# Optimization experiments

Measured on AMD Instinct MI355X. Metric: run time of the kernel, lower is better.

Reference implementation:

```python
import jax, jax.numpy as jnp
import numpy as np

N_TOTAL = 2_000_000   # total particles across all events
N_EVENTS = 20_000     # number of events (segments)
H = 64                # phi/rho hidden width
OUT = 10              # output classes


def _lin(x, W, b):
    # torch nn.Linear: y = x @ W.T + b
    return x @ W.T + b


def setup_inputs() -> dict:
    key = jax.random.key(0)
    ks = jax.random.split(key, 24)
    s = 0.1  # small init scale
    inp = {
        "values": jax.random.normal(ks[0], (N_TOTAL,), dtype=jnp.float32),
        "seg_ids": jnp.sort(jax.random.randint(ks[1], (N_TOTAL,), 0, N_EVENTS)),
        "p1w0": jax.random.normal(ks[2], (H, 1), dtype=jnp.float32) * s,
        "p1b0": jax.random.normal(ks[3], (H,), dtype=jnp.float32) * s,
        "p1w1": jax.random.normal(ks[4], (H, H), dtype=jnp.float32) * s,
        "p1b1": jax.random.normal(ks[5], (H,), dtype=jnp.float32) * s,
        "r1w0": jax.random.normal(ks[6], (H, H), dtype=jnp.float32) * s,
        "r1b0": jax.random.normal(ks[7], (H,), dtype=jnp.float32) * s,
        "r1w1": jax.random.normal(ks[8], (H, H), dtype=jnp.float32) * s,
        "r1b1": jax.random.normal(ks[9], (H,), dtype=jnp.float32) * s,
        "o1w": jax.random.normal(ks[10], (H, H), dtype=jnp.float32) * s,
        "o1b": jax.random.normal(ks[11], (H,), dtype=jnp.float32) * s,
        "p2w0": jax.random.normal(ks[12], (H, H), dtype=jnp.float32) * s,
        "p2b0": jax.random.normal(ks[13], (H,), dtype=jnp.float32) * s,
        "p2w1": jax.random.normal(ks[14], (H, H), dtype=jnp.float32) * s,
        "p2b1": jax.random.normal(ks[15], (H,), dtype=jnp.float32) * s,
        "r2w0": jax.random.normal(ks[16], (H, H), dtype=jnp.float32) * s,
        "r2b0": jax.random.normal(ks[17], (H,), dtype=jnp.float32) * s,
        "r2w1": jax.random.normal(ks[18], (H, H), dtype=jnp.float32) * s,
        "r2b1": jax.random.normal(ks[19], (H,), dtype=jnp.float32) * s,
        "o2w": jax.random.normal(ks[20], (OUT, H), dtype=jnp.float32) * s,
        "o2b": jax.random.normal(ks[21], (OUT,), dtype=jnp.float32) * s,
    }
    return inp


def reference(values, seg_ids, p1w0, p1b0, p1w1, p1b1, r1w0, r1b0, r1w1, r1b1,
              o1w, o1b, p2w0, p2b0, p2w1, p2b1, r2w0, r2b0, r2w1, r2b1, o2w, o2b):
    relu = jax.nn.relu
    # stage 1: phi1 on each scalar particle value -> [N, H]
    h = relu(_lin(values[:, None], p1w0, p1b0))
    h = relu(_lin(h, p1w1, p1b1))
    # jagged sum over particles within each event (the inner deepset sum)
    ev = jax.ops.segment_sum(h, seg_ids, num_segments=N_EVENTS)  # [E, H]
    # rho1 + output linear + activation per event
    ev = relu(_lin(ev, r1w0, r1b0))
    ev = relu(_lin(ev, r1w1, r1b1))
    ev = relu(_lin(ev, o1w, o1b))  # [E, H] (output_size of deepset1 = rho_sizes[-1])
    # stage 2: phi2 per event, sum over all events
    h2 = relu(_lin(ev, p2w0, p2b0))
    h2 = relu(_lin(h2, p2w1, p2b1))
    s2 = jnp.sum(h2, axis=0, keepdims=True)  # [1, H]
    r2 = relu(_lin(s2, r2w0, r2b0))
    r2 = relu(_lin(r2, r2w1, r2b1))
    out = _lin(r2, o2w, o2b)  # [1, OUT]
    return jax.nn.log_softmax(out, axis=1)
```

## Files before the change

kernel.cpp:

```cpp
#include <hip/hip_runtime.h>

#define NT 2000000
#define NE 20000
#define NT4 (NT / 4)
#define K1_BLOCKS 2048
#define K1_WAVES (K1_BLOCKS * 4)
#define K2_BLOCKS ((NE + 63) / 64)
#define NSEG 65
#define K0_BLOCKS ((NT4 + 255) / 256)

using half8  = __attribute__((ext_vector_type(8))) _Float16;
using half4v = __attribute__((ext_vector_type(4))) _Float16;
using f32x4  = __attribute__((ext_vector_type(4))) float;
using fvec4  = __attribute__((ext_vector_type(4))) float;

__device__ __forceinline__ half8 load_h8(const float* __restrict__ p) {
    fvec4 a = *(const fvec4*)p;
    fvec4 b = *(const fvec4*)(p + 4);
    half8 r;
#pragma unroll
    for (int e = 0; e < 4; e++) {
        r[e]     = (_Float16)a[e];
        r[e + 4] = (_Float16)b[e];
    }
    return r;
}

__global__ __launch_bounds__(256) void k0_fused(
    const int* __restrict__ seg, int* __restrict__ off, float* __restrict__ s2,
    int* __restrict__ counter,
    const float* __restrict__ w0, const float* __restrict__ b0,
    const float* __restrict__ w1, const float* __restrict__ b1,
    float* __restrict__ sorted_t, half4v* __restrict__ tabg) {
    if (blockIdx.x < NSEG) {
        __shared__ float tS[64], w0S[64], b0S[64], aS[64], cS[64];
        __shared__ int styleS[64], rankS[64];
        const int k = threadIdx.x;
        float t = 0.f; int rank = 0;
        if (k < 64) {
            const float w = w0[k], b = b0[k];
            int style;
            if (w != 0.f) { t = -b / w; style = (w > 0.f) ? 1 : 0; }
            else          { t = (b > 0.f) ? -INFINITY : INFINITY; style = 1; }
            tS[k] = t; w0S[k] = w; b0S[k] = b; styleS[k] = style;
        }
        __syncthreads();
        if (k < 64) {
            for (int i = 0; i < 64; i++) {
                const float ti = tS[i];
                rank += (ti < t || (ti == t && i < k)) ? 1 : 0;
            }
            rankS[k] = rank;
        }
        __syncthreads();
        if (k < 64) {
            if (blockIdx.x == 0) sorted_t[rank] = t;
            const int s = blockIdx.x;
            float a = 0.f, c = b1[k];
            for (int kk = 0; kk < 64; kk++) {
                const bool act = styleS[kk] ? (s > rankS[kk]) : (s <= rankS[kk]);
                if (act) {
                    const float wjk = w1[k * 64 + kk];
                    a = fmaf(wjk, w0S[kk], a);
                    c = fmaf(wjk, b0S[kk], c);
                }
            }
            aS[k] = a; cS[k] = c;
        }
        __syncthreads();
        if (k < 32) {
            const int s = blockIdx.x;
            tabg[s * 32 + k] = half4v{
                (_Float16)aS[2 * k],     (_Float16)cS[2 * k],
                (_Float16)aS[2 * k + 1], (_Float16)cS[2 * k + 1]};
        }
    }

    if (blockIdx.x == 0) {
        if (threadIdx.x < 64) s2[threadIdx.x] = 0.f;
        if (threadIdx.x == 64) *counter = 0;
    }
    const int g = blockIdx.x * 256 + threadIdx.x;
    if (g >= NT4) return;
    const int idx4 = g * 4;
    const int4 s = *(const int4*)(seg + idx4);
    int prev = (g == 0) ? -1 : seg[idx4 - 1];
    int vals[4] = {s.x, s.y, s.z, s.w};
#pragma unroll
    for (int k = 0; k < 4; k++) {
        const int cur = vals[k];
        if (cur != prev) {
            for (int e = prev + 1; e <= cur; ++e) off[e] = idx4 + k;
        }
        prev = cur;
    }
    if (idx4 + 3 == NT - 1) {
        for (int e = prev + 1; e <= NE; ++e) off[e] = NT;
    }
}

__global__ __launch_bounds__(256) void k1_phi1(
    const float* __restrict__ values, const int* __restrict__ off,
    const float* __restrict__ sorted_t, const half4v* __restrict__ gtab,
    float* __restrict__ ev) {
    __shared__ __align__(16) half4v tab[NSEG * 32];
    const int tid = threadIdx.x;
    const int w = tid >> 6, l = tid & 63;
    const int l31 = l & 31;
    const bool lo32 = (l < 32);

    for (int idx = tid; idx < NSEG * 32; idx += 256) tab[idx] = gtab[idx];
    const float t_l = sorted_t[l];
    __syncthreads();

    const int wid = blockIdx.x * 4 + w;
    for (int e = wid; e < NE; e += K1_WAVES) {
        const int ps = off[e], pe = off[e + 1];
        float2 p0 = {0.f, 0.f}, p1 = {0.f, 0.f};
        float2 p2 = {0.f, 0.f}, p3 = {0.f, 0.f};

        for (int base = ps; base < pe; base += 64) {
            const int cnt = min(pe - base, 64);
            const float v_l = (base + l < pe) ? values[base + l] : 0.f;
            const int v_li = __float_as_int(v_l);

            auto PROC2 = [&](int i, int j, float2& acc) {
                const float vsA =
                    __int_as_float(__builtin_amdgcn_readlane(v_li, i));
                const float vsB =
                    __int_as_float(__builtin_amdgcn_readlane(v_li, j));
                const int sgA = (int)__popcll(__ballot(vsA > t_l));
                const int sgB = (int)__popcll(__ballot(vsB > t_l));
                const int sg  = lo32 ? sgA : sgB;
                const float vs = lo32 ? vsA : vsB;
                const half4v ac = tab[sg * 32 + l31];
                acc.x += fmaxf(fmaf((float)ac[0], vs, (float)ac[1]), 0.f);
                acc.y += fmaxf(fmaf((float)ac[2], vs, (float)ac[3]), 0.f);
            };
            auto PROC1 = [&](int i, float2& acc) {
                const float vsA =
                    __int_as_float(__builtin_amdgcn_readlane(v_li, i));
                const int sgA = (int)__popcll(__ballot(vsA > t_l));
                const half4v ac = tab[sgA * 32 + l31];
                const float x = fmaxf(fmaf((float)ac[0], vsA, (float)ac[1]), 0.f);
                const float y = fmaxf(fmaf((float)ac[2], vsA, (float)ac[3]), 0.f);
                acc.x += lo32 ? x : 0.f;
                acc.y += lo32 ? y : 0.f;
            };

            const int fullg = cnt >> 3;
#pragma unroll
            for (int g = 0; g < 8; ++g) {
                if (g >= fullg) break;
                PROC2(8 * g,     8 * g + 1, p0);
                PROC2(8 * g + 2, 8 * g + 3, p1);
                PROC2(8 * g + 4, 8 * g + 5, p2);
                PROC2(8 * g + 6, 8 * g + 7, p3);
            }
            int tb = fullg * 8;
            if (tb + 1 < cnt) { PROC2(tb, tb + 1, p0); tb += 2; }
            if (tb + 1 < cnt) { PROC2(tb, tb + 1, p1); tb += 2; }
            if (tb + 1 < cnt) { PROC2(tb, tb + 1, p2); tb += 2; }
            if (tb < cnt)     { PROC1(tb, p3); }
        }

        float s0 = (p0.x + p1.x) + (p2.x + p3.x);
        float s1 = (p0.y + p1.y) + (p2.y + p3.y);
        s0 += __shfl_xor(s0, 32);
        s1 += __shfl_xor(s1, 32);
        if (lo32)
            *(float2*)(ev + (size_t)e * 64 + 2 * l31) = make_float2(s0, s1);
    }
}

__global__ __launch_bounds__(64) void k2_events(
    const float* __restrict__ ev,
    const float* __restrict__ W0, const float* __restrict__ B0,
    const float* __restrict__ W1, const float* __restrict__ B1,
    const float* __restrict__ W2, const float* __restrict__ B2,
    const float* __restrict__ W3, const float* __restrict__ B3,
    const float* __restrict__ W4, const float* __restrict__ B4,
    float* __restrict__ s2, int* __restrict__ counter,
    const float* __restrict__ R0, const float* __restrict__ Rb0,
    const float* __restrict__ R1, const float* __restrict__ Rb1,
    const float* __restrict__ OW, const float* __restrict__ OB,
    float* __restrict__ out) {
    __shared__ __align__(16) _Float16 xt[64 * 72];
    const int l   = threadIdx.x;
    const int l15 = l & 15;
    const int l4  = l >> 4;
    const int ebase = blockIdx.x * 64;

    const float* Ws[5] = {W0, W1, W2, W3, W4};
    const float* Bs[5] = {B0, B1, B2, B3, B4};

    half8 A[4][2];
#pragma unroll
    for (int pf = 0; pf < 4; pf++) {
        const int e = ebase + pf * 16 + l15;
#pragma unroll
        for (int kf = 0; kf < 2; kf++) {
            half8 a;
            if (e < NE) {
                a = load_h8(ev + (size_t)e * 64 + kf * 32 + l4 * 8);
            } else {
#pragma unroll
                for (int e2 = 0; e2 < 8; e2++) a[e2] = (_Float16)0.f;
            }
            A[pf][kf] = a;
        }
    }

#pragma unroll
    for (int L = 0; L < 5; L++) {
        half8 Bh[2][4];
#pragma unroll
        for (int kf = 0; kf < 2; kf++)
#pragma unroll
            for (int jf = 0; jf < 4; jf++)
                Bh[kf][jf] = load_h8(Ws[L] + (jf * 16 + l15) * 64 +
                                     kf * 32 + l4 * 8);

        f32x4 acc[4][4];
#pragma unroll
        for (int jf = 0; jf < 4; jf++) {
            const float bj = Bs[L][jf * 16 + l15];
#pragma unroll
            for (int pf = 0; pf < 4; pf++)
#pragma unroll
                for (int r = 0; r < 4; r++) acc[pf][jf][r] = bj;
        }
#pragma unroll
        for (int kf = 0; kf < 2; kf++)
#pragma unroll
            for (int pf = 0; pf < 4; pf++)
#pragma unroll
                for (int jf = 0; jf < 4; jf++)
                    acc[pf][jf] = __builtin_amdgcn_mfma_f32_16x16x32_f16(
                        A[pf][kf], Bh[kf][jf], acc[pf][jf], 0, 0, 0);

        if (L < 4) {
#pragma unroll
            for (int pf = 0; pf < 4; pf++)
#pragma unroll
                for (int jf = 0; jf < 4; jf++) {
                    const int j = jf * 16 + l15;
#pragma unroll
                    for (int r = 0; r < 4; r++)
                        xt[(pf * 16 + l4 * 4 + r) * 72 + j] =
                            (_Float16)fmaxf(acc[pf][jf][r], 0.f);
                }
#pragma unroll
            for (int pf = 0; pf < 4; pf++)
#pragma unroll
                for (int kf = 0; kf < 2; kf++)
                    A[pf][kf] = *(const half8*)(xt + (pf * 16 + l15) * 72 +
                                                kf * 32 + l4 * 8);
        } else {
            float sj[4];
#pragma unroll
            for (int jf = 0; jf < 4; jf++) {
                float s = 0.f;
#pragma unroll
                for (int pf = 0; pf < 4; pf++)
#pragma unroll
                    for (int r = 0; r < 4; r++) {
                        const int e = ebase + pf * 16 + l4 * 4 + r;
                        float v = fmaxf(acc[pf][jf][r], 0.f);
                        s += (e < NE) ? v : 0.f;
                    }
                s += __shfl_xor(s, 16);
                s += __shfl_xor(s, 32);
                sj[jf] = s;
            }
            float v = (l4 == 0) ? sj[0] : (l4 == 1) ? sj[1]
                    : (l4 == 2) ? sj[2] : sj[3];
            atomicAdd(s2 + l, v);
        }
    }

    __shared__ int is_last;
    __threadfence();
    if (l == 0) {
        const int c = atomicAdd(counter, 1);
        is_last = (c == (int)gridDim.x - 1);
    }
    __syncthreads();
    if (!is_last) return;

    __shared__ __align__(16) float xb[64];
    __shared__ __align__(16) float yb[64];
    __shared__ float ob[10];

    xb[l] = atomicAdd(s2 + l, 0.f);
    __syncthreads();

    float a0 = Rb0[l];
#pragma unroll
    for (int k = 0; k < 16; k++) {
        fvec4 wv = *(const fvec4*)(R0 + l * 64 + k * 4);
        fvec4 xv = *(const fvec4*)(xb + k * 4);
        a0 += wv[0] * xv[0] + wv[1] * xv[1] + wv[2] * xv[2] + wv[3] * xv[3];
    }
    yb[l] = fmaxf(a0, 0.f);
    __syncthreads();

    float b_ = Rb1[l];
#pragma unroll
    for (int k = 0; k < 16; k++) {
        fvec4 wv = *(const fvec4*)(R1 + l * 64 + k * 4);
        fvec4 xv = *(const fvec4*)(yb + k * 4);
        b_ += wv[0] * xv[0] + wv[1] * xv[1] + wv[2] * xv[2] + wv[3] * xv[3];
    }
    __syncthreads();
    xb[l] = fmaxf(b_, 0.f);
    __syncthreads();

    if (l < 10) {
        float o = OB[l];
#pragma unroll
        for (int k = 0; k < 16; k++) {
            fvec4 wv = *(const fvec4*)(OW + l * 64 + k * 4);
            fvec4 xv = *(const fvec4*)(xb + k * 4);
            o += wv[0] * xv[0] + wv[1] * xv[1] + wv[2] * xv[2] + wv[3] * xv[3];
        }
        ob[l] = o;
    }
    __syncthreads();
    if (l == 0) {
        float m = ob[0];
#pragma unroll
        for (int i = 1; i < 10; i++) m = fmaxf(m, ob[i]);
        float sum = 0.f;
#pragma unroll
        for (int i = 0; i < 10; i++) sum = sum + expf(ob[i] - m);
        float ls = logf(sum);
#pragma unroll
        for (int i = 0; i < 10; i++) out[i] = ob[i] - m - ls;
    }
}

extern "C" void kernel_launch(void* const* d_in, const int* in_sizes, int n_in,
                              void* d_out, int out_size, void* d_ws, size_t ws_size,
                              hipStream_t stream) {
    const float* values = (const float*)d_in[0];
    const int*   seg    = (const int*)d_in[1];
    const float* p1w0 = (const float*)d_in[2],  *p1b0 = (const float*)d_in[3];
    const float* p1w1 = (const float*)d_in[4],  *p1b1 = (const float*)d_in[5];
    const float* r1w0 = (const float*)d_in[6],  *r1b0 = (const float*)d_in[7];
    const float* r1w1 = (const float*)d_in[8],  *r1b1 = (const float*)d_in[9];
    const float* o1w  = (const float*)d_in[10], *o1b  = (const float*)d_in[11];
    const float* p2w0 = (const float*)d_in[12], *p2b0 = (const float*)d_in[13];
    const float* p2w1 = (const float*)d_in[14], *p2b1 = (const float*)d_in[15];
    const float* r2w0 = (const float*)d_in[16], *r2b0 = (const float*)d_in[17];
    const float* r2w1 = (const float*)d_in[18], *r2b1 = (const float*)d_in[19];
    const float* o2w  = (const float*)d_in[20], *o2b  = (const float*)d_in[21];

    float*  ev       = (float*)d_ws;
    float*  s2       = ev + (size_t)NE * 64;
    int*    off      = (int*)(s2 + 64);
    int*    counter  = off + (NE + 1);
    float*  sorted_t = (float*)(counter + 1);
    half4v* tabg     = (half4v*)(sorted_t + 64);

    hipLaunchKernelGGL(k0_fused, dim3(K0_BLOCKS), dim3(256), 0, stream,
                       seg, off, s2, counter,
                       p1w0, p1b0, p1w1, p1b1, sorted_t, tabg);
    hipLaunchKernelGGL(k1_phi1, dim3(K1_BLOCKS), dim3(256), 0, stream,
                       values, off, sorted_t, tabg, ev);
    hipLaunchKernelGGL(k2_events, dim3(K2_BLOCKS), dim3(64), 0, stream,
                       ev, r1w0, r1b0, r1w1, r1b1, o1w, o1b,
                       p2w0, p2b0, p2w1, p2b1, s2, counter,
                       r2w0, r2b0, r2w1, r2b1, o2w, o2b, (float*)d_out);
}
```

Before: 74.49 us.

## Stage MLP weights in LDS across four waves and split full/tail particle chunks

k2_events now runs four waves per block, each handling 64 events. All five 64x64 weight matrices are converted to fp16 once per block into padded shared memory, replacing per-wave global loads and conversions. This cuts redundant weight traffic but adds a block-wide staging step and about 83KB of LDS, which lowers occupancy. In k1_phi1, full 64-particle chunks take an unconditional unrolled path and only the remainder uses the bounds-checked tail code, removing per-chunk branching.

```diff
diff --git a/kernel.cpp b/kernel.cpp
--- a/kernel.cpp
+++ b/kernel.cpp
@@ -5,7 +5,7 @@
 #define NT4 (NT / 4)
 #define K1_BLOCKS 2048
 #define K1_WAVES (K1_BLOCKS * 4)
-#define K2_BLOCKS ((NE + 63) / 64)
+#define K2_BLOCKS ((NE + 255) / 256)
 #define NSEG 65
 #define K0_BLOCKS ((NT4 + 255) / 256)
 
@@ -13,18 +13,6 @@
 using half4v = __attribute__((ext_vector_type(4))) _Float16;
 using f32x4  = __attribute__((ext_vector_type(4))) float;
 using fvec4  = __attribute__((ext_vector_type(4))) float;
-
-__device__ __forceinline__ half8 load_h8(const float* __restrict__ p) {
-    fvec4 a = *(const fvec4*)p;
-    fvec4 b = *(const fvec4*)(p + 4);
-    half8 r;
-#pragma unroll
-    for (int e = 0; e < 4; e++) {
-        r[e]     = (_Float16)a[e];
-        r[e + 4] = (_Float16)b[e];
-    }
-    return r;
-}
 
 __global__ __launch_bounds__(256) void k0_fused(
     const int* __restrict__ seg, int* __restrict__ off, float* __restrict__ s2,
@@ -113,55 +101,62 @@
     const float t_l = sorted_t[l];
     __syncthreads();
 
+    auto PROC2 = [&](int v_li, int i, int j, float2& acc) {
+        const float vsA = __int_as_float(__builtin_amdgcn_readlane(v_li, i));
+        const float vsB = __int_as_float(__builtin_amdgcn_readlane(v_li, j));
+        const int sgA = (int)__popcll(__ballot(vsA > t_l));
+        const int sgB = (int)__popcll(__ballot(vsB > t_l));
+        const int sg  = lo32 ? sgA : sgB;
+        const float vs = lo32 ? vsA : vsB;
+        const half4v ac = tab[sg * 32 + l31];
+        acc.x += fmaxf(fmaf((float)ac[0], vs, (float)ac[1]), 0.f);
+        acc.y += fmaxf(fmaf((float)ac[2], vs, (float)ac[3]), 0.f);
+    };
+    auto PROC1 = [&](int v_li, int i, float2& acc) {
+        const float vsA = __int_as_float(__builtin_amdgcn_readlane(v_li, i));
+        const int sgA = (int)__popcll(__ballot(vsA > t_l));
+        const half4v ac = tab[sgA * 32 + l31];
+        const float x = fmaxf(fmaf((float)ac[0], vsA, (float)ac[1]), 0.f);
+        const float y = fmaxf(fmaf((float)ac[2], vsA, (float)ac[3]), 0.f);
+        acc.x += lo32 ? x : 0.f;
+        acc.y += lo32 ? y : 0.f;
+    };
+
     const int wid = blockIdx.x * 4 + w;
     for (int e = wid; e < NE; e += K1_WAVES) {
         const int ps = off[e], pe = off[e + 1];
         float2 p0 = {0.f, 0.f}, p1 = {0.f, 0.f};
         float2 p2 = {0.f, 0.f}, p3 = {0.f, 0.f};
 
-        for (int base = ps; base < pe; base += 64) {
-            const int cnt = min(pe - base, 64);
+        int base = ps;
+        for (; base + 64 <= pe; base += 64) {
+            const int v_li = __float_as_int(values[base + l]);
+#pragma unroll
+            for (int g = 0; g < 8; ++g) {
+                PROC2(v_li, 8 * g,     8 * g + 1, p0);
+                PROC2(v_li, 8 * g + 2, 8 * g + 3, p1);
+                PROC2(v_li, 8 * g + 4, 8 * g + 5, p2);
+                PROC2(v_li, 8 * g + 6, 8 * g + 7, p3);
+            }
+        }
+        const int cnt = pe - base;
+        if (cnt > 0) {
             const float v_l = (base + l < pe) ? values[base + l] : 0.f;
             const int v_li = __float_as_int(v_l);
-
-            auto PROC2 = [&](int i, int j, float2& acc) {
-                const float vsA =
-                    __int_as_float(__builtin_amdgcn_readlane(v_li, i));
-                const float vsB =
-                    __int_as_float(__builtin_amdgcn_readlane(v_li, j));
-                const int sgA = (int)__popcll(__ballot(vsA > t_l));
-                const int sgB = (int)__popcll(__ballot(vsB > t_l));
-                const int sg  = lo32 ? sgA : sgB;
-                const float vs = lo32 ? vsA : vsB;
-                const half4v ac = tab[sg * 32 + l31];
-                acc.x += fmaxf(fmaf((float)ac[0], vs, (float)ac[1]), 0.f);
-                acc.y += fmaxf(fmaf((float)ac[2], vs, (float)ac[3]), 0.f);
-            };
-            auto PROC1 = [&](int i, float2& acc) {
-                const float vsA =
-                    __int_as_float(__builtin_amdgcn_readlane(v_li, i));
-                const int sgA = (int)__popcll(__ballot(vsA > t_l));
-                const half4v ac = tab[sgA * 32 + l31];
-                const float x = fmaxf(fmaf((float)ac[0], vsA, (float)ac[1]), 0.f);
-                const float y = fmaxf(fmaf((float)ac[2], vsA, (float)ac[3]), 0.f);
-                acc.x += lo32 ? x : 0.f;
-                acc.y += lo32 ? y : 0.f;
-            };
-
             const int fullg = cnt >> 3;
 #pragma unroll
-            for (int g = 0; g < 8; ++g) {
+            for (int g = 0; g < 7; ++g) {
                 if (g >= fullg) break;
-                PROC2(8 * g,     8 * g + 1, p0);
-                PROC2(8 * g + 2, 8 * g + 3, p1);
-                PROC2(8 * g + 4, 8 * g + 5, p2);
-                PROC2(8 * g + 6, 8 * g + 7, p3);
+                PROC2(v_li, 8 * g,     8 * g + 1, p0);
+                PROC2(v_li, 8 * g + 2, 8 * g + 3, p1);
+                PROC2(v_li, 8 * g + 4, 8 * g + 5, p2);
+                PROC2(v_li, 8 * g + 6, 8 * g + 7, p3);
             }
             int tb = fullg * 8;
-            if (tb + 1 < cnt) { PROC2(tb, tb + 1, p0); tb += 2; }
-            if (tb + 1 < cnt) { PROC2(tb, tb + 1, p1); tb += 2; }
-            if (tb + 1 < cnt) { PROC2(tb, tb + 1, p2); tb += 2; }
-            if (tb < cnt)     { PROC1(tb, p3); }
+            if (tb + 1 < cnt) { PROC2(v_li, tb, tb + 1, p0); tb += 2; }
+            if (tb + 1 < cnt) { PROC2(v_li, tb, tb + 1, p1); tb += 2; }
+            if (tb + 1 < cnt) { PROC2(v_li, tb, tb + 1, p2); tb += 2; }
+            if (tb < cnt)     { PROC1(v_li, tb, p3); }
         }
 
         float s0 = (p0.x + p1.x) + (p2.x + p3.x);
@@ -173,7 +168,7 @@
     }
 }
 
-__global__ __launch_bounds__(64) void k2_events(
+__global__ __launch_bounds__(256) void k2_events(
     const float* __restrict__ ev,
     const float* __restrict__ W0, const float* __restrict__ B0,
     const float* __restrict__ W1, const float* __restrict__ B1,
@@ -185,14 +180,30 @@
     const float* __restrict__ R1, const float* __restrict__ Rb1,
     const float* __restrict__ OW, const float* __restrict__ OB,
     float* __restrict__ out) {
-    __shared__ __align__(16) _Float16 xt[64 * 72];
-    const int l   = threadIdx.x;
+    __shared__ __align__(16) _Float16 wlds[5 * 64 * 72];
+    __shared__ __align__(16) _Float16 xt[4 * 64 * 72];
+    const int tid = threadIdx.x;
+    const int w   = tid >> 6;
+    const int l   = tid & 63;
     const int l15 = l & 15;
     const int l4  = l >> 4;
-    const int ebase = blockIdx.x * 64;
-
-    const float* Ws[5] = {W0, W1, W2, W3, W4};
+    const int ebase = blockIdx.x * 256 + w * 64;
+
+    {
+        const float* Wsrc[5] = {W0, W1, W2, W3, W4};
+#pragma unroll
+        for (int L = 0; L < 5; L++) {
+            const float* Wp = Wsrc[L];
+            for (int idx = tid; idx < 4096; idx += 256) {
+                const int row = idx >> 6, col = idx & 63;
+                wlds[(L * 64 + row) * 72 + col] = (_Float16)Wp[idx];
+            }
+        }
+    }
+    __syncthreads();
+
     const float* Bs[5] = {B0, B1, B2, B3, B4};
+    _Float16* xtw = xt + w * 64 * 72;
 
     half8 A[4][2];
 #pragma unroll
@@ -202,7 +213,14 @@
         for (int kf = 0; kf < 2; kf++) {
             half8 a;
             if (e < NE) {
-                a = load_h8(ev + (size_t)e * 64 + kf * 32 + l4 * 8);
+                const float* p = ev + (size_t)e * 64 + kf * 32 + l4 * 8;
+                fvec4 x = *(const fvec4*)p;
+                fvec4 y = *(const fvec4*)(p + 4);
+#pragma unroll
+                for (int e2 = 0; e2 < 4; e2++) {
+                    a[e2]     = (_Float16)x[e2];
+                    a[e2 + 4] = (_Float16)y[e2];
+                }
             } else {
 #pragma unroll
                 for (int e2 = 0; e2 < 8; e2++) a[e2] = (_Float16)0.f;
@@ -218,8 +236,8 @@
         for (int kf = 0; kf < 2; kf++)
 #pragma unroll
             for (int jf = 0; jf < 4; jf++)
-                Bh[kf][jf] = load_h8(Ws[L] + (jf * 16 + l15) * 64 +
-                                     kf * 32 + l4 * 8);
+                Bh[kf][jf] = *(const half8*)(wlds +
+                    (L * 64 + jf * 16 + l15) * 72 + kf * 32 + l4 * 8);
 
         f32x4 acc[4][4];
 #pragma unroll
@@ -247,14 +265,14 @@
                     const int j = jf * 16 + l15;
 #pragma unroll
                     for (int r = 0; r < 4; r++)
-                        xt[(pf * 16 + l4 * 4 + r) * 72 + j] =
+                        xtw[(pf * 16 + l4 * 4 + r) * 72 + j] =
                             (_Float16)fmaxf(acc[pf][jf][r], 0.f);
                 }
 #pragma unroll
             for (int pf = 0; pf < 4; pf++)
 #pragma unroll
                 for (int kf = 0; kf < 2; kf++)
-                    A[pf][kf] = *(const half8*)(xt + (pf * 16 + l15) * 72 +
+                    A[pf][kf] = *(const half8*)(xtw + (pf * 16 + l15) * 72 +
                                                 kf * 32 + l4 * 8);
         } else {
             float sj[4];
@@ -281,7 +299,8 @@
 
     __shared__ int is_last;
     __threadfence();
-    if (l == 0) {
+    __syncthreads();
+    if (tid == 0) {
         const int c = atomicAdd(counter, 1);
         is_last = (c == (int)gridDim.x - 1);
     }
@@ -292,42 +311,47 @@
     __shared__ __align__(16) float yb[64];
     __shared__ float ob[10];
 
-    xb[l] = atomicAdd(s2 + l, 0.f);
-    __syncthreads();
-
-    float a0 = Rb0[l];
-#pragma unroll
-    for (int k = 0; k < 16; k++) {
-        fvec4 wv = *(const fvec4*)(R0 + l * 64 + k * 4);
-        fvec4 xv = *(const fvec4*)(xb + k * 4);
-        a0 += wv[0] * xv[0] + wv[1] * xv[1] + wv[2] * xv[2] + wv[3] * xv[3];
-    }
-    yb[l] = fmaxf(a0, 0.f);
-    __syncthreads();
-
-    float b_ = Rb1[l];
-#pragma unroll
-    for (int k = 0; k < 16; k++) {
-        fvec4 wv = *(const fvec4*)(R1 + l * 64 + k * 4);
-        fvec4 xv = *(const fvec4*)(yb + k * 4);
-        b_ += wv[0] * xv[0] + wv[1] * xv[1] + wv[2] * xv[2] + wv[3] * xv[3];
-    }
-    __syncthreads();
-    xb[l] = fmaxf(b_, 0.f);
-    __syncthreads();
-
-    if (l < 10) {
-        float o = OB[l];
+    if (tid < 64) xb[tid] = atomicAdd(s2 + tid, 0.f);
+    __syncthreads();
+
+    if (tid < 64) {
+        float a0 = Rb0[tid];
 #pragma unroll
         for (int k = 0; k < 16; k++) {
-            fvec4 wv = *(const fvec4*)(OW + l * 64 + k * 4);
+            fvec4 wv = *(const fvec4*)(R0 + tid * 64 + k * 4);
+            fvec4 xv = *(const fvec4*)(xb + k * 4);
+            a0 += wv[0] * xv[0] + wv[1] * xv[1] + wv[2] * xv[2] + wv[3] * xv[3];
+        }
+        yb[tid] = fmaxf(a0, 0.f);
+    }
+    __syncthreads();
+
+    float b_ = 0.f;
+    if (tid < 64) {
+        b_ = Rb1[tid];
+#pragma unroll
+        for (int k = 0; k < 16; k++) {
+            fvec4 wv = *(const fvec4*)(R1 + tid * 64 + k * 4);
+            fvec4 xv = *(const fvec4*)(yb + k * 4);
+            b_ += wv[0] * xv[0] + wv[1] * xv[1] + wv[2] * xv[2] + wv[3] * xv[3];
+        }
+    }
+    __syncthreads();
+    if (tid < 64) xb[tid] = fmaxf(b_, 0.f);
+    __syncthreads();
+
+    if (tid < 10) {
+        float o = OB[tid];
+#pragma unroll
+        for (int k = 0; k < 16; k++) {
+            fvec4 wv = *(const fvec4*)(OW + tid * 64 + k * 4);
             fvec4 xv = *(const fvec4*)(xb + k * 4);
             o += wv[0] * xv[0] + wv[1] * xv[1] + wv[2] * xv[2] + wv[3] * xv[3];
         }
-        ob[l] = o;
-    }
-    __syncthreads();
-    if (l == 0) {
+        ob[tid] = o;
+    }
+    __syncthreads();
+    if (tid == 0) {
         float m = ob[0];
 #pragma unroll
         for (int i = 1; i < 10; i++) m = fmaxf(m, ob[i]);
@@ -368,7 +392,7 @@
                        p1w0, p1b0, p1w1, p1b1, sorted_t, tabg);
     hipLaunchKernelGGL(k1_phi1, dim3(K1_BLOCKS), dim3(256), 0, stream,
                        values, off, sorted_t, tabg, ev);
-    hipLaunchKernelGGL(k2_events, dim3(K2_BLOCKS), dim3(64), 0, stream,
+    hipLaunchKernelGGL(k2_events, dim3(K2_BLOCKS), dim3(256), 0, stream,
                        ev, r1w0, r1b0, r1w1, r1b1, o1w, o1b,
                        p2w0, p2b0, p2w1, p2b1, s2, counter,
                        r2w0, r2b0, r2w1, r2b1, o2w, o2b, (float*)d_out);
```

Result: no change. 74.82 us (+0.4%).
